# Kernel optimization log

Measured on AMD Instinct MI355X. Metric: run time of the kernel, lower is better.

## Reference

```python
import jax, jax.numpy as jnp
import numpy as np

NUM_HEADS = 16
VALUE_SIZE = 64
MODEL_SIZE = 1024
BATCH = 4
SEQ = 1024


def setup_inputs() -> dict:
    key = jax.random.key(0)
    ks = jax.random.split(key, 5)
    scale = 1.0 / np.sqrt(MODEL_SIZE)
    x = jax.random.normal(ks[0], (BATCH, SEQ, MODEL_SIZE), dtype=jnp.float32)
    w_q = jax.random.normal(ks[1], (MODEL_SIZE, NUM_HEADS * VALUE_SIZE), dtype=jnp.float32) * scale
    w_kv = jax.random.normal(ks[2], (MODEL_SIZE, NUM_HEADS * VALUE_SIZE), dtype=jnp.float32) * scale
    w_o = jax.random.normal(ks[3], (NUM_HEADS * VALUE_SIZE, MODEL_SIZE), dtype=jnp.float32) * scale
    # original init is Constant(0.0); use small random values for a non-trivial test
    k_weights = jax.random.normal(ks[4], (1, NUM_HEADS, 1, VALUE_SIZE), dtype=jnp.float32) * 0.02
    return {"x": x, "w_q": w_q, "w_kv": w_kv, "w_o": w_o, "k_weights": k_weights}


def reference(x, w_q, w_kv, w_o, k_weights):
    b, L, d = x.shape
    h, v = NUM_HEADS, VALUE_SIZE
    # projections (no bias); q scaled by 1/sqrt(model_size)
    q = (x @ w_q) * (1.0 / jnp.sqrt(jnp.asarray(d, x.dtype)))
    q = q.reshape(b, L, h, v).transpose(0, 2, 1, 3)    # b h l v
    kv = (x @ w_kv).reshape(b, L, h, v).transpose(0, 2, 1, 3)  # b h l v
    # learned per-head key scaling on the shared k=v tensor
    k = kv * (1.0 + k_weights)
    logits = jnp.einsum('bhik,bhjk->bhij', q, k)       # b h L L
    mask = jnp.tril(jnp.ones((L, L), dtype=bool))
    logits = jnp.where(mask, logits, jnp.asarray(-1e6, logits.dtype))
    a = jax.nn.softmax(logits, axis=-1)
    y = jnp.einsum('bhij,bhjv->bhiv', a, kv)           # attend over shared kv
    y = y.transpose(0, 2, 1, 3).reshape(b, L, h * v)
    return y @ w_o
```

## Files before the change

kernel.cpp:

```cpp
#include <hip/hip_runtime.h>
#include <hip/hip_bf16.h>
#include <stdint.h>

#define BATCH 4
#define SEQ   1024
#define DMODEL 1024
#define NH    16
#define DV    64

typedef short bf8 __attribute__((ext_vector_type(8)));
typedef float f4  __attribute__((ext_vector_type(4)));

static __device__ __forceinline__ short f2bf(float f) {
    union { float f; uint32_t u; } a; a.f = f;
    uint32_t r = a.u + 0x7FFF + ((a.u >> 16) & 1);
    return (short)(r >> 16);
}

static __device__ __forceinline__ f4 mfma16(bf8 a, bf8 b, f4 c) {
    return __builtin_amdgcn_mfma_f32_16x16x32_bf16(a, b, c, 0, 0, 0);
}

static __device__ __forceinline__ void gload16(const short* g, short* l) {
    __builtin_amdgcn_global_load_lds((const __attribute__((address_space(1))) void*)g,
                                     (__attribute__((address_space(3))) void*)l,
                                     16, 0, 0);
}


__global__ void prep_kernel(const float* __restrict__ x,
                            const float* __restrict__ wq, const float* __restrict__ wkv,
                            const float* __restrict__ wo,
                            short* __restrict__ xb,
                            short* __restrict__ wqkvt, short* __restrict__ wot) {
    int z = blockIdx.z;
    int tx = threadIdx.x, ty = threadIdx.y;
    if (z >= 3) {
        int i = (((z - 3) * 1024 + blockIdx.y * 32 + blockIdx.x) << 8) + ty * 32 + tx;
        float4 v = ((const float4*)x)[i];
        short4 o;
        o.x = f2bf(v.x); o.y = f2bf(v.y); o.z = f2bf(v.z); o.w = f2bf(v.w);
        ((short4*)xb)[i] = o;
        return;
    }
    __shared__ float tile[32][33];
    const float* w = (z == 0) ? wq : (z == 1) ? wkv : wo;
    short* wt = (z == 0) ? wqkvt : (z == 1) ? (wqkvt + (1u << 20)) : wot;
    int bx = blockIdx.x, by = blockIdx.y;
    #pragma unroll
    for (int i = 0; i < 4; i++)
        tile[ty + i * 8][tx] = w[(size_t)(by * 32 + ty + i * 8) * 1024 + bx * 32 + tx];
    __syncthreads();
    #pragma unroll
    for (int i = 0; i < 4; i++)
        wt[(size_t)(bx * 32 + ty + i * 8) * 1024 + by * 32 + tx] = f2bf(tile[tx][ty + i * 8]);
}


__global__ __launch_bounds__(256) void gemm_proj_kernel(
    const short* __restrict__ A, const short* __restrict__ Bt,
    const float* __restrict__ kw,
    short* __restrict__ q_out, short* __restrict__ kv_out, short* __restrict__ kvT_out)
{
    __shared__ short SM[32768];
    const int K = DMODEL;

    int tid = threadIdx.x;
    int wave = tid >> 6, lane = tid & 63;
    int quad = lane >> 4, l16 = lane & 15;

    int flat = blockIdx.x + (blockIdx.y << 4);
    int xcd = flat & 7, pos = flat >> 3;
    int nby = ((xcd >> 1) << 3) + (pos >> 3);
    int nbx = ((xcd & 1) << 3) + (pos & 7);
    int m0 = nby * 128;
    int n0 = nbx * 128;

    int wm = (wave >> 1) * 64;
    int wn = (wave & 1) * 64;
    int sw = l16 & 7;

    f4 acc[4][4] = {};

    auto stage = [&](int buf, int k0) {
        short* As = SM + buf * 16384;
        short* Bs = As + 8192;
        #pragma unroll
        for (int c = 0; c < 4; c++) {
            int flt = c * 256 + tid;
            int row = flt >> 3;
            int seg = (flt & 7) ^ (row & 7);
            gload16(A + (size_t)(m0 + row) * K + k0 + seg * 8, As + flt * 8);
        }
        #pragma unroll
        for (int c = 0; c < 4; c++) {
            int flt = c * 256 + tid;
            int row = flt >> 3;
            int seg = (flt & 7) ^ (row & 7);
            gload16(Bt + (size_t)(n0 + row) * K + k0 + seg * 8, Bs + flt * 8);
        }
    };

    stage(0, 0);
    for (int k0 = 0; k0 < K; k0 += 64) {
        int buf = (k0 >> 6) & 1;
        __syncthreads();
        if (k0 + 64 < K) stage(buf ^ 1, k0 + 64);
        const short* As = SM + buf * 16384;
        const short* Bs = As + 8192;
        #pragma unroll
        for (int kk = 0; kk < 2; kk++) {
            bf8 ar[4], br[4];
            #pragma unroll
            for (int i = 0; i < 4; i++)
                ar[i] = *(const bf8*)(As + (wm + i * 16 + l16) * 64 + ((kk * 4 + quad) ^ sw) * 8);
            #pragma unroll
            for (int j = 0; j < 4; j++)
                br[j] = *(const bf8*)(Bs + (wn + j * 16 + l16) * 64 + ((kk * 4 + quad) ^ sw) * 8);
            #pragma unroll
            for (int i = 0; i < 4; i++) {
                #pragma unroll
                for (int j = 0; j < 4; j++)
                    acc[i][j] = mfma16(ar[i], br[j], acc[i][j]);
            }
        }
    }

    if (n0 < 1024) {
        #pragma unroll
        for (int j = 0; j < 4; j++) {
            int n = n0 + wn + j * 16 + l16;
            float kws = 0.03125f * (1.0f + kw[n]);
            #pragma unroll
            for (int i = 0; i < 4; i++) {
                int mb = m0 + wm + i * 16 + quad * 4;
                q_out[(size_t)(mb + 0) * 1024 + n] = f2bf(acc[i][j][0] * kws);
                q_out[(size_t)(mb + 1) * 1024 + n] = f2bf(acc[i][j][1] * kws);
                q_out[(size_t)(mb + 2) * 1024 + n] = f2bf(acc[i][j][2] * kws);
                q_out[(size_t)(mb + 3) * 1024 + n] = f2bf(acc[i][j][3] * kws);
            }
        }
        return;
    }

    #pragma unroll
    for (int j = 0; j < 4; j++) {
        int n2 = n0 - 1024 + wn + j * 16 + l16;
        #pragma unroll
        for (int i = 0; i < 4; i++) {
            int mb = m0 + wm + i * 16 + quad * 4;
            kv_out[(size_t)(mb + 0) * 1024 + n2] = f2bf(acc[i][j][0]);
            kv_out[(size_t)(mb + 1) * 1024 + n2] = f2bf(acc[i][j][1]);
            kv_out[(size_t)(mb + 2) * 1024 + n2] = f2bf(acc[i][j][2]);
            kv_out[(size_t)(mb + 3) * 1024 + n2] = f2bf(acc[i][j][3]);
        }
    }

    {
        const int TST = 136;
        short* T = SM;
        __syncthreads();
        short* Tw = T + (wave & 1) * (64 * TST);
        #pragma unroll
        for (int j = 0; j < 4; j++) {
            int nl = j * 16 + l16;
            #pragma unroll
            for (int i = 0; i < 4; i++) {
                short4 tv;
                tv.x = f2bf(acc[i][j][0]); tv.y = f2bf(acc[i][j][1]);
                tv.z = f2bf(acc[i][j][2]); tv.w = f2bf(acc[i][j][3]);
                *(short4*)(Tw + nl * TST + wm + i * 16 + quad * 4) = tv;
            }
        }
        __syncthreads();
        int n2base = n0 - 1024;
        int mloc = m0 & 1023;
        int bq = m0 >> 10;
        #pragma unroll
        for (int c = 0; c < 8; c++) {
            int flt = c * 256 + tid;
            int row = flt >> 4;
            int seg = flt & 15;
            bf8 vseg = *(const bf8*)(T + (row >> 6) * (64 * TST) + (row & 63) * TST + seg * 8);
            int n2 = n2base + row;
            int bh = (bq << 4) + (n2 >> 6);
            *(bf8*)(kvT_out + (size_t)(bh * 64 + (n2 & 63)) * 1024 + mloc + seg * 8) = vseg;
        }
    }
}


__global__ __launch_bounds__(256) void gemm_out_kernel(
    const short* __restrict__ A, const short* __restrict__ Bt,
    float* __restrict__ c_out)
{
    __shared__ short SM[32768];
    const int K = DMODEL;

    int tid = threadIdx.x;
    int wave = tid >> 6, lane = tid & 63;
    int quad = lane >> 4, l16 = lane & 15;

    int flat = blockIdx.x + (blockIdx.y << 3);
    int xcd = flat & 7, pos = flat >> 3;
    int nby = ((xcd >> 1) << 3) + (pos >> 2);
    int nbx = ((xcd & 1) << 2) + (pos & 3);
    int m0 = nby * 128;
    int n0 = nbx * 128;

    int wm = (wave >> 1) * 64;
    int wn = (wave & 1) * 64;
    int sw = l16 & 7;

    f4 acc[4][4] = {};

    auto stage = [&](int buf, int k0) {
        short* As = SM + buf * 16384;
        short* Bs = As + 8192;
        #pragma unroll
        for (int c = 0; c < 4; c++) {
            int flt = c * 256 + tid;
            int row = flt >> 3;
            int seg = (flt & 7) ^ (row & 7);
            gload16(A + (size_t)(m0 + row) * K + k0 + seg * 8, As + flt * 8);
        }
        #pragma unroll
        for (int c = 0; c < 4; c++) {
            int flt = c * 256 + tid;
            int row = flt >> 3;
            int seg = (flt & 7) ^ (row & 7);
            gload16(Bt + (size_t)(n0 + row) * K + k0 + seg * 8, Bs + flt * 8);
        }
    };

    stage(0, 0);
    for (int k0 = 0; k0 < K; k0 += 64) {
        int buf = (k0 >> 6) & 1;
        __syncthreads();
        if (k0 + 64 < K) stage(buf ^ 1, k0 + 64);
        const short* As = SM + buf * 16384;
        const short* Bs = As + 8192;
        #pragma unroll
        for (int kk = 0; kk < 2; kk++) {
            bf8 ar[4], br[4];
            #pragma unroll
            for (int i = 0; i < 4; i++)
                ar[i] = *(const bf8*)(As + (wm + i * 16 + l16) * 64 + ((kk * 4 + quad) ^ sw) * 8);
            #pragma unroll
            for (int j = 0; j < 4; j++)
                br[j] = *(const bf8*)(Bs + (wn + j * 16 + l16) * 64 + ((kk * 4 + quad) ^ sw) * 8);
            #pragma unroll
            for (int i = 0; i < 4; i++) {
                #pragma unroll
                for (int j = 0; j < 4; j++)
                    acc[i][j] = mfma16(ar[i], br[j], acc[i][j]);
            }
        }
    }

    #pragma unroll
    for (int j = 0; j < 4; j++) {
        int n = n0 + wn + j * 16 + l16;
        #pragma unroll
        for (int i = 0; i < 4; i++) {
            int mb = m0 + wm + i * 16 + quad * 4;
            c_out[(size_t)(mb + 0) * 1024 + n] = acc[i][j][0];
            c_out[(size_t)(mb + 1) * 1024 + n] = acc[i][j][1];
            c_out[(size_t)(mb + 2) * 1024 + n] = acc[i][j][2];
            c_out[(size_t)(mb + 3) * 1024 + n] = acc[i][j][3];
        }
    }
}


#define PLD 72

__global__ __launch_bounds__(256) void attn_kernel(
    const short* __restrict__ qg, const short* __restrict__ kvg,
    const short* __restrict__ kvTg, short* __restrict__ yg)
{
    int bh = blockIdx.y;
    int b = bh >> 4, h = bh & 15;
    int x = blockIdx.x;
    int tid = threadIdx.x;
    int wave = tid >> 6, lane = tid & 63;
    int quad = lane >> 4, l16 = lane & 15;
    int qa0 = x * 64;
    int qb0 = (15 - x) * 64;
    int ntiles = 16 - x;

    __shared__ short Ks[2][64 * 64];
    __shared__ short Vs[2][64 * 64];
    __shared__ short Ps[4][2 * 16 * PLD];
    short* myPB = &Ps[wave][0];
    short* myPA = &Ps[wave][16 * PLD];

    const short* qpa = qg + (size_t)(b * 1024 + qa0 + wave * 16 + l16) * 1024 + h * 64;
    const short* qpb = qg + (size_t)(b * 1024 + qb0 + wave * 16 + l16) * 1024 + h * 64;
    bf8 qa_0 = *(const bf8*)(qpa + quad * 8);
    bf8 qa_1 = *(const bf8*)(qpa + 32 + quad * 8);
    bf8 qb_0 = *(const bf8*)(qpb + quad * 8);
    bf8 qb_1 = *(const bf8*)(qpb + 32 + quad * 8);

    bf8 ones;
    #pragma unroll
    for (int j = 0; j < 8; j++) ones[j] = (short)0x3F80;

    f4 oa[4] = {}, ob[4] = {};
    f4 lsa = {}, lsb = {};
    int rowbaseA = qa0 + wave * 16 + quad * 4;
    int rowbaseB = qb0 + wave * 16 + quad * 4;

    auto stage = [&](int jt) {
        short* dstK = &Ks[jt & 1][0];
        short* dstV = &Vs[jt & 1][0];
        int j0 = jt * 64;
        #pragma unroll
        for (int k = 0; k < 2; k++) {
            int flat = k * 256 + tid;
            int row = flat >> 3;
            int lseg = (flat & 7) ^ (row & 7);
            gload16(kvg + (size_t)(b * 1024 + j0 + row) * 1024 + h * 64 + lseg * 8,
                    dstK + flat * 8);
            gload16(kvTg + (size_t)(bh * 64 + row) * 1024 + j0 + lseg * 8,
                    dstV + flat * 8);
        }
    };

    auto qk = [&](bf8 qf0, bf8 qf1, const short* K, f4 (&s)[4]) {
        #pragma unroll
        for (int c = 0; c < 4; c++) {
            int row = c * 16 + l16;
            int swz = row & 7;
            bf8 kb0 = *(const bf8*)(K + row * 64 + (quad ^ swz) * 8);
            bf8 kb1 = *(const bf8*)(K + row * 64 + (((quad + 4) ^ swz)) * 8);
            f4 t = {};
            t = mfma16(qf0, kb0, t);
            t = mfma16(qf1, kb1, t);
            s[c] = t;
        }
    };

    auto expstoreU = [&](f4 (&s)[4], short* P) {
        #pragma unroll
        for (int r = 0; r < 4; r++) {
            int prow = quad * 4 + r;
            P[prow * PLD + l16]      = f2bf(__expf(s[0][r]));
            P[prow * PLD + 16 + l16] = f2bf(__expf(s[1][r]));
            P[prow * PLD + 32 + l16] = f2bf(__expf(s[2][r]));
            P[prow * PLD + 48 + l16] = f2bf(__expf(s[3][r]));
        }
    };

    auto expstoreM = [&](f4 (&s)[4], int rowbase, int j0, short* P) {
        #pragma unroll
        for (int r = 0; r < 4; r++) {
            int qi = rowbase + r;
            float p0 = (j0 + l16      <= qi) ? __expf(s[0][r]) : 0.0f;
            float p1 = (j0 + 16 + l16 <= qi) ? __expf(s[1][r]) : 0.0f;
            float p2 = (j0 + 32 + l16 <= qi) ? __expf(s[2][r]) : 0.0f;
            float p3 = (j0 + 48 + l16 <= qi) ? __expf(s[3][r]) : 0.0f;
            int prow = quad * 4 + r;
            P[prow * PLD + l16]      = f2bf(p0);
            P[prow * PLD + 16 + l16] = f2bf(p1);
            P[prow * PLD + 32 + l16] = f2bf(p2);
            P[prow * PLD + 48 + l16] = f2bf(p3);
        }
    };

    auto pv = [&](const short* P, const short* V, f4 (&o)[4], f4& lsum) {
        bf8 pf0 = *(const bf8*)(P + l16 * PLD + quad * 8);
        bf8 pf1 = *(const bf8*)(P + l16 * PLD + 32 + quad * 8);
        lsum = mfma16(pf0, ones, lsum);
        lsum = mfma16(pf1, ones, lsum);
        #pragma unroll
        for (int t = 0; t < 4; t++) {
            int vrow = t * 16 + l16;
            int swz = vrow & 7;
            bf8 vb0 = *(const bf8*)(V + vrow * 64 + (quad ^ swz) * 8);
            bf8 vb1 = *(const bf8*)(V + vrow * 64 + (((quad + 4) ^ swz)) * 8);
            o[t] = mfma16(pf0, vb0, o[t]);
            o[t] = mfma16(pf1, vb1, o[t]);
        }
    };

    stage(0);

    for (int jt = 0; jt < ntiles; jt++) {
        __syncthreads();
        if (jt + 1 < ntiles) stage(jt + 1);
        const short* K = &Ks[jt & 1][0];
        const short* V = &Vs[jt & 1][0];
        int j0 = jt * 64;
        bool doA = (jt <= x);

        if (doA) {
            f4 sb[4], sa[4];
            #pragma unroll
            for (int c = 0; c < 4; c++) {
                int row = c * 16 + l16;
                int swz = row & 7;
                bf8 kb0 = *(const bf8*)(K + row * 64 + (quad ^ swz) * 8);
                bf8 kb1 = *(const bf8*)(K + row * 64 + (((quad + 4) ^ swz)) * 8);
                f4 tb = {};
                tb = mfma16(qb_0, kb0, tb);
                tb = mfma16(qb_1, kb1, tb);
                sb[c] = tb;
                f4 ta = {};
                ta = mfma16(qa_0, kb0, ta);
                ta = mfma16(qa_1, kb1, ta);
                sa[c] = ta;
            }
            expstoreU(sb, myPB);
            if (jt == x) expstoreM(sa, rowbaseA, j0, myPA);
            else         expstoreU(sa, myPA);
            bf8 pb0 = *(const bf8*)(myPB + l16 * PLD + quad * 8);
            bf8 pb1 = *(const bf8*)(myPB + l16 * PLD + 32 + quad * 8);
            bf8 pa0 = *(const bf8*)(myPA + l16 * PLD + quad * 8);
            bf8 pa1 = *(const bf8*)(myPA + l16 * PLD + 32 + quad * 8);
            lsb = mfma16(pb0, ones, lsb);
            lsb = mfma16(pb1, ones, lsb);
            lsa = mfma16(pa0, ones, lsa);
            lsa = mfma16(pa1, ones, lsa);
            #pragma unroll
            for (int t = 0; t < 4; t++) {
                int vrow = t * 16 + l16;
                int swz = vrow & 7;
                bf8 vb0 = *(const bf8*)(V + vrow * 64 + (quad ^ swz) * 8);
                bf8 vb1 = *(const bf8*)(V + vrow * 64 + (((quad + 4) ^ swz)) * 8);
                ob[t] = mfma16(pb0, vb0, ob[t]);
                ob[t] = mfma16(pb1, vb1, ob[t]);
                oa[t] = mfma16(pa0, vb0, oa[t]);
                oa[t] = mfma16(pa1, vb1, oa[t]);
            }
        } else {
            f4 sb[4];
            qk(qb_0, qb_1, K, sb);
            if (jt == ntiles - 1) expstoreM(sb, rowbaseB, j0, myPB);
            else                  expstoreU(sb, myPB);
            pv(myPB, V, ob, lsb);
        }
    }

    {
        float r0 = 1.0f / lsa[0], r1 = 1.0f / lsa[1], r2 = 1.0f / lsa[2], r3 = 1.0f / lsa[3];
        #pragma unroll
        for (int t = 0; t < 4; t++) {
            size_t base = (size_t)(b * SEQ + rowbaseA) * (NH * DV) + h * DV + t * 16 + l16;
            yg[base]                 = f2bf(oa[t][0] * r0);
            yg[base + 1 * (NH * DV)] = f2bf(oa[t][1] * r1);
            yg[base + 2 * (NH * DV)] = f2bf(oa[t][2] * r2);
            yg[base + 3 * (NH * DV)] = f2bf(oa[t][3] * r3);
        }
    }
    {
        float r0 = 1.0f / lsb[0], r1 = 1.0f / lsb[1], r2 = 1.0f / lsb[2], r3 = 1.0f / lsb[3];
        #pragma unroll
        for (int t = 0; t < 4; t++) {
            size_t base = (size_t)(b * SEQ + rowbaseB) * (NH * DV) + h * DV + t * 16 + l16;
            yg[base]                 = f2bf(ob[t][0] * r0);
            yg[base + 1 * (NH * DV)] = f2bf(ob[t][1] * r1);
            yg[base + 2 * (NH * DV)] = f2bf(ob[t][2] * r2);
            yg[base + 3 * (NH * DV)] = f2bf(ob[t][3] * r3);
        }
    }
}


extern "C" void kernel_launch(void* const* d_in, const int* in_sizes, int n_in,
                              void* d_out, int out_size, void* d_ws, size_t ws_size,
                              hipStream_t stream) {
    const float* x    = (const float*)d_in[0];
    const float* w_q  = (const float*)d_in[1];
    const float* w_kv = (const float*)d_in[2];
    const float* w_o  = (const float*)d_in[3];
    const float* kw   = (const float*)d_in[4];
    float* out = (float*)d_out;

    char* ws = (char*)d_ws;
    short* xb    = (short*)(ws);
    short* wqkvt = (short*)(ws + ( 8u << 20));
    short* wot   = (short*)(ws + (12u << 20));
    short* qp    = (short*)(ws + (14u << 20));
    short* kvb   = (short*)(ws + (22u << 20));
    short* kvT   = (short*)(ws + (30u << 20));
    short* yb    = (short*)(ws + (38u << 20));

    prep_kernel<<<dim3(32, 32, 7), dim3(32, 8), 0, stream>>>(
        x, w_q, w_kv, w_o, xb, wqkvt, wot);

    gemm_proj_kernel<<<dim3(16, 32), 256, 0, stream>>>(
        xb, wqkvt, kw, qp, kvb, kvT);

    attn_kernel<<<dim3(8, BATCH * NH), 256, 0, stream>>>(qp, kvb, kvT, yb);

    gemm_out_kernel<<<dim3(8, 32), 256, 0, stream>>>(yb, wot, out);
}
```

Baseline: 147.9 us.

## Replace paired causal query tiles with one query tile per block

```diff
diff --git a/kernel.cpp b/kernel.cpp
--- a/kernel.cpp
+++ b/kernel.cpp
@@ -281,35 +281,29 @@
 {
     int bh = blockIdx.y;
     int b = bh >> 4, h = bh & 15;
-    int x = blockIdx.x;
+    int qt = 15 - blockIdx.x;
     int tid = threadIdx.x;
     int wave = tid >> 6, lane = tid & 63;
     int quad = lane >> 4, l16 = lane & 15;
-    int qa0 = x * 64;
-    int qb0 = (15 - x) * 64;
-    int ntiles = 16 - x;
+    int qa0 = qt * 64;
+    int ntiles = qt + 1;
 
     __shared__ short Ks[2][64 * 64];
     __shared__ short Vs[2][64 * 64];
-    __shared__ short Ps[4][2 * 16 * PLD];
-    short* myPB = &Ps[wave][0];
-    short* myPA = &Ps[wave][16 * PLD];
+    __shared__ short Ps[4][16 * PLD];
+    short* myP = &Ps[wave][0];
 
     const short* qpa = qg + (size_t)(b * 1024 + qa0 + wave * 16 + l16) * 1024 + h * 64;
-    const short* qpb = qg + (size_t)(b * 1024 + qb0 + wave * 16 + l16) * 1024 + h * 64;
     bf8 qa_0 = *(const bf8*)(qpa + quad * 8);
     bf8 qa_1 = *(const bf8*)(qpa + 32 + quad * 8);
-    bf8 qb_0 = *(const bf8*)(qpb + quad * 8);
-    bf8 qb_1 = *(const bf8*)(qpb + 32 + quad * 8);
 
     bf8 ones;
     #pragma unroll
     for (int j = 0; j < 8; j++) ones[j] = (short)0x3F80;
 
-    f4 oa[4] = {}, ob[4] = {};
-    f4 lsa = {}, lsb = {};
-    int rowbaseA = qa0 + wave * 16 + quad * 4;
-    int rowbaseB = qb0 + wave * 16 + quad * 4;
+    f4 oa[4] = {};
+    f4 lsa = {};
+    int rowbase = qa0 + wave * 16 + quad * 4;
 
     auto stage = [&](int jt) {
         short* dstK = &Ks[jt & 1][0];
@@ -327,7 +321,7 @@
         }
     };
 
-    auto qk = [&](bf8 qf0, bf8 qf1, const short* K, f4 (&s)[4]) {
+    auto qk = [&](const short* K, f4 (&s)[4]) {
         #pragma unroll
         for (int c = 0; c < 4; c++) {
             int row = c * 16 + l16;
@@ -335,8 +329,8 @@
             bf8 kb0 = *(const bf8*)(K + row * 64 + (quad ^ swz) * 8);
             bf8 kb1 = *(const bf8*)(K + row * 64 + (((quad + 4) ^ swz)) * 8);
             f4 t = {};
-            t = mfma16(qf0, kb0, t);
-            t = mfma16(qf1, kb1, t);
+            t = mfma16(qa_0, kb0, t);
+            t = mfma16(qa_1, kb1, t);
             s[c] = t;
         }
     };
@@ -352,7 +346,7 @@
         }
     };
 
-    auto expstoreM = [&](f4 (&s)[4], int rowbase, int j0, short* P) {
+    auto expstoreM = [&](f4 (&s)[4], int j0, short* P) {
         #pragma unroll
         for (int r = 0; r < 4; r++) {
             int qi = rowbase + r;
@@ -368,19 +362,19 @@
         }
     };
 
-    auto pv = [&](const short* P, const short* V, f4 (&o)[4], f4& lsum) {
+    auto pv = [&](const short* P, const short* V) {
         bf8 pf0 = *(const bf8*)(P + l16 * PLD + quad * 8);
         bf8 pf1 = *(const bf8*)(P + l16 * PLD + 32 + quad * 8);
-        lsum = mfma16(pf0, ones, lsum);
-        lsum = mfma16(pf1, ones, lsum);
+        lsa = mfma16(pf0, ones, lsa);
+        lsa = mfma16(pf1, ones, lsa);
         #pragma unroll
         for (int t = 0; t < 4; t++) {
             int vrow = t * 16 + l16;
             int swz = vrow & 7;
             bf8 vb0 = *(const bf8*)(V + vrow * 64 + (quad ^ swz) * 8);
             bf8 vb1 = *(const bf8*)(V + vrow * 64 + (((quad + 4) ^ swz)) * 8);
-            o[t] = mfma16(pf0, vb0, o[t]);
-            o[t] = mfma16(pf1, vb1, o[t]);
+            oa[t] = mfma16(pf0, vb0, oa[t]);
+            oa[t] = mfma16(pf1, vb1, oa[t]);
         }
     };
 
@@ -392,76 +386,23 @@
         const short* K = &Ks[jt & 1][0];
         const short* V = &Vs[jt & 1][0];
         int j0 = jt * 64;
-        bool doA = (jt <= x);
-
-        if (doA) {
-            f4 sb[4], sa[4];
-            #pragma unroll
-            for (int c = 0; c < 4; c++) {
-                int row = c * 16 + l16;
-                int swz = row & 7;
-                bf8 kb0 = *(const bf8*)(K + row * 64 + (quad ^ swz) * 8);
-                bf8 kb1 = *(const bf8*)(K + row * 64 + (((quad + 4) ^ swz)) * 8);
-                f4 tb = {};
-                tb = mfma16(qb_0, kb0, tb);
-                tb = mfma16(qb_1, kb1, tb);
-                sb[c] = tb;
-                f4 ta = {};
-                ta = mfma16(qa_0, kb0, ta);
-                ta = mfma16(qa_1, kb1, ta);
-                sa[c] = ta;
-            }
-            expstoreU(sb, myPB);
-            if (jt == x) expstoreM(sa, rowbaseA, j0, myPA);
-            else         expstoreU(sa, myPA);
-            bf8 pb0 = *(const bf8*)(myPB + l16 * PLD + quad * 8);
-            bf8 pb1 = *(const bf8*)(myPB + l16 * PLD + 32 + quad * 8);
-            bf8 pa0 = *(const bf8*)(myPA + l16 * PLD + quad * 8);
-            bf8 pa1 = *(const bf8*)(myPA + l16 * PLD + 32 + quad * 8);
-            lsb = mfma16(pb0, ones, lsb);
-            lsb = mfma16(pb1, ones, lsb);
-            lsa = mfma16(pa0, ones, lsa);
-            lsa = mfma16(pa1, ones, lsa);
-            #pragma unroll
-            for (int t = 0; t < 4; t++) {
-                int vrow = t * 16 + l16;
-                int swz = vrow & 7;
-                bf8 vb0 = *(const bf8*)(V + vrow * 64 + (quad ^ swz) * 8);
-                bf8 vb1 = *(const bf8*)(V + vrow * 64 + (((quad + 4) ^ swz)) * 8);
-                ob[t] = mfma16(pb0, vb0, ob[t]);
-                ob[t] = mfma16(pb1, vb1, ob[t]);
-                oa[t] = mfma16(pa0, vb0, oa[t]);
-                oa[t] = mfma16(pa1, vb1, oa[t]);
-            }
-        } else {
-            f4 sb[4];
-            qk(qb_0, qb_1, K, sb);
-            if (jt == ntiles - 1) expstoreM(sb, rowbaseB, j0, myPB);
-            else                  expstoreU(sb, myPB);
-            pv(myPB, V, ob, lsb);
-        }
+
+        f4 sa[4];
+        qk(K, sa);
+        if (jt == qt) expstoreM(sa, j0, myP);
+        else          expstoreU(sa, myP);
+        pv(myP, V);
     }
 
     {
         float r0 = 1.0f / lsa[0], r1 = 1.0f / lsa[1], r2 = 1.0f / lsa[2], r3 = 1.0f / lsa[3];
         #pragma unroll
         for (int t = 0; t < 4; t++) {
-            size_t base = (size_t)(b * SEQ + rowbaseA) * (NH * DV) + h * DV + t * 16 + l16;
+            size_t base = (size_t)(b * SEQ + rowbase) * (NH * DV) + h * DV + t * 16 + l16;
             yg[base]                 = f2bf(oa[t][0] * r0);
             yg[base + 1 * (NH * DV)] = f2bf(oa[t][1] * r1);
             yg[base + 2 * (NH * DV)] = f2bf(oa[t][2] * r2);
             yg[base + 3 * (NH * DV)] = f2bf(oa[t][3] * r3);
-        }
-    }
-    {
-        float r0 = 1.0f / lsb[0], r1 = 1.0f / lsb[1], r2 = 1.0f / lsb[2], r3 = 1.0f / lsb[3];
-        #pragma unroll
-        for (int t = 0; t < 4; t++) {
-            size_t base = (size_t)(b * SEQ + rowbaseB) * (NH * DV) + h * DV + t * 16 + l16;
-            yg[base]                 = f2bf(ob[t][0] * r0);
-            yg[base + 1 * (NH * DV)] = f2bf(ob[t][1] * r1);
-            yg[base + 2 * (NH * DV)] = f2bf(ob[t][2] * r2);
-            yg[base + 3 * (NH * DV)] = f2bf(ob[t][3] * r3);
         }
     }
 }
@@ -492,7 +433,7 @@
     gemm_proj_kernel<<<dim3(16, 32), 256, 0, stream>>>(
         xb, wqkvt, kw, qp, kvb, kvT);
 
-    attn_kernel<<<dim3(8, BATCH * NH), 256, 0, stream>>>(qp, kvb, kvT, yb);
+    attn_kernel<<<dim3(16, BATCH * NH), 256, 0, stream>>>(qp, kvb, kvT, yb);
 
     gemm_out_kernel<<<dim3(8, 32), 256, 0, stream>>>(yb, wot, out);
 }
```

Result: slower. 157.9 us (+6.8%).
